# Kernel optimization log

Measured on AMD Instinct MI355X. Metric: run time of the kernel, lower is better.

## Reference

```python
import jax, jax.numpy as jnp
import numpy as np

N, C, H, W = 4, 128, 64, 64


def setup_inputs() -> dict:
    key = jax.random.key(0)
    ks = jax.random.split(key, 4)
    s = 1.0 / np.sqrt(C).astype(np.float32)  # conv2d default-init scale
    return {
        "x": jax.random.normal(ks[0], (N, C, H, W), dtype=jnp.float32),
        "Wq": jax.random.normal(ks[1], (C, C), dtype=jnp.float32) * s,
        "bq": jnp.zeros((C,), dtype=jnp.float32),
        "Wk": jax.random.normal(ks[2], (C, C), dtype=jnp.float32) * s,
        "bk": jnp.zeros((C,), dtype=jnp.float32),
        "Wv": jax.random.normal(ks[3], (C, C), dtype=jnp.float32) * s,
        "bv": jnp.zeros((C,), dtype=jnp.float32),
    }


def reference(x, Wq, bq, Wk, bk, Wv, bv):
    n, c, h, w = x.shape
    xf = x.reshape(n, c, h * w)  # [N, C, L], L = H*W
    # 1x1 convs == per-pixel channel mixing
    q = jnp.einsum('oc,ncl->nol', Wq, xf) + bq[:, None]
    k = jnp.einsum('oc,ncl->nol', Wk, xf) + bk[:, None]
    v = jnp.einsum('oc,ncl->nol', Wv, xf) + bv[:, None]
    # scores[l, m] = sum_c k[c,l] * q[c,m]  (matmul(k^T, q))
    scale = jnp.asarray(1.0 / np.sqrt(c), x.dtype)
    scores = jnp.einsum('ncl,ncm->nlm', k, q) * scale  # [N, L, L]
    temp = jax.nn.softmax(scores, axis=-1)
    attn = jnp.einsum('ncl,nlm->ncm', v, temp)  # [N, C, L]
    return x + attn.reshape(n, c, h, w)
```

## Files before the change

kernel.cpp:

```cpp
#include <hip/hip_runtime.h>
#include <hip/hip_bf16.h>
#include <stdint.h>

#define NB 4
#define CH 128
#define LL 4096

typedef __attribute__((ext_vector_type(8))) short short8;
typedef __attribute__((ext_vector_type(4))) short short4b;
typedef __attribute__((ext_vector_type(4))) float floatx4;
typedef __attribute__((ext_vector_type(16))) float floatx16;


static __device__ __forceinline__ short f2bf(float f) {
    uint32_t u = __float_as_uint(f);
    u += 0x7fffu + ((u >> 16) & 1u);
    return (short)(u >> 16);
}

__global__ __launch_bounds__(256) void wprep_kernel(
    const float* __restrict__ Wq, const float* __restrict__ Wk,
    const float* __restrict__ Wv, short* __restrict__ Wf)
{
    const int g = blockIdx.x * 256 + threadIdx.x;
    const int mat = g >> 14;
    const int rem = g & 16383;
    const int o   = rem >> 7;
    const int c   = rem & 127;
    const float* W = (mat == 0) ? Wq : (mat == 1) ? Wk : Wv;
    float v = W[o * CH + c];
    if (mat == 1) v *= 0.08838834764831845f;
    Wf[(size_t)mat * 16384 + (o >> 4) * 2048 + (c >> 5) * 512
       + ((c >> 3) & 3) * 128 + (o & 15) * 8 + (c & 7)] = f2bf(v);
}

__global__ __launch_bounds__(256) void proj_kernel(
    const float* __restrict__ x, const short* __restrict__ Wf,
    const float* __restrict__ bq, const float* __restrict__ bk,
    const float* __restrict__ bv,
    short* __restrict__ Qf, short* __restrict__ Kf, short* __restrict__ Vp)
{
    const int b    = blockIdx.x;
    const int n    = b >> 7;
    const int lt   = b & 127;
    const int l0   = lt << 5;
    const int tid  = threadIdx.x;
    const int wave = tid >> 6;
    const int lane = tid & 63;
    const int quad = lane >> 4;
    const int mc   = lane & 15;

    __shared__ short Xb[32][136];

    {
        const int sl = tid & 31;
        const int cg = tid >> 5;
        const float* xp = x + ((size_t)n * CH + cg * 16) * LL + l0 + sl;
        short8 buf;
        #pragma unroll
        for (int i = 0; i < 16; ++i) {
            buf[i & 7] = f2bf(xp[(size_t)i * LL]);
            if ((i & 7) == 7)
                *(short8*)(void*)&Xb[sl][cg * 16 + (i & 8)] = buf;
        }
    }
    __syncthreads();

    const int lt2 = wave >> 1;
    const int oh  = wave & 1;
    const int gt  = lt * 2 + lt2;

    short8 xf[4];
    #pragma unroll
    for (int s = 0; s < 4; ++s)
        xf[s] = *(const short8*)(const void*)&Xb[lt2 * 16 + mc][32 * s + quad * 8];

    const size_t obase = ((size_t)n * 256 + gt) * 2048;

    #pragma unroll
    for (int mat = 0; mat < 3; ++mat) {
        const short* Wm = Wf + (size_t)mat * 16384;
        const float* bb = (mat == 0) ? bq : (mat == 1) ? bk : bv;
        const float bscale = (mat == 1) ? 0.08838834764831845f : 1.0f;
        #pragma unroll
        for (int ot = oh * 4; ot < oh * 4 + 4; ++ot) {
            floatx4 acc = {0.f, 0.f, 0.f, 0.f};
            #pragma unroll
            for (int s = 0; s < 4; ++s)
                acc = __builtin_amdgcn_mfma_f32_16x16x32_bf16(
                    *(const short8*)(const void*)(Wm + ot * 2048 + s * 512 + lane * 8),
                    xf[s], acc, 0, 0, 0);
            const int c0 = ot * 16 + 4 * quad;
            if (mat < 2) {
                short4b pv;
                #pragma unroll
                for (int r = 0; r < 4; ++r)
                    pv[r] = f2bf(acc[r] + bb[c0 + r] * bscale);
                short* dst = ((mat == 0) ? Qf : Kf) + obase
                           + (c0 >> 5) * 512 + ((c0 >> 3) & 3) * 128
                           + mc * 8 + (c0 & 7);
                *(short4b*)(void*)dst = pv;
            } else {
                #pragma unroll
                for (int r = 0; r < 4; ++r)
                    Vp[obase + (c0 + r) * 16 + mc] = f2bf(acc[r] + bb[c0 + r]);
            }
        }
    }
}

__global__ __launch_bounds__(256) void rowsum_kernel(
    const short* __restrict__ Qf, const short* __restrict__ Kf,
    float* __restrict__ Dsum)
{
    const int b    = blockIdx.x;
    const int n    = b >> 7;
    const int tp   = b & 127;
    const int wave = threadIdx.x >> 6;
    const int lane = threadIdx.x & 63;
    const int quad = lane >> 4;
    const int mc   = lane & 15;

    const short* Kb = Kf + ((size_t)n * 256 + tp * 2) * 2048 + lane * 8;
    short8 kf[2][4];
    #pragma unroll
    for (int t = 0; t < 2; ++t)
        #pragma unroll
        for (int s = 0; s < 4; ++s)
            kf[t][s] = *(const short8*)(const void*)(Kb + t * 2048 + s * 512);

    const short* Qn = Qf + (size_t)n * 524288 + (size_t)wave * 64 * 2048 + lane * 8;
    float rs[2][4] = {{0.f,0.f,0.f,0.f},{0.f,0.f,0.f,0.f}};

    for (int i = 0; i < 64; i += 2) {
        floatx4 a[2][2];
        #pragma unroll
        for (int t = 0; t < 2; ++t)
            #pragma unroll
            for (int j = 0; j < 2; ++j) a[t][j] = (floatx4){0.f,0.f,0.f,0.f};
        #pragma unroll
        for (int s = 0; s < 4; ++s) {
            const short8 q0 = *(const short8*)(const void*)(Qn + (size_t)i * 2048 + s * 512);
            const short8 q1 = *(const short8*)(const void*)(Qn + (size_t)(i + 1) * 2048 + s * 512);
            #pragma unroll
            for (int t = 0; t < 2; ++t) {
                a[t][0] = __builtin_amdgcn_mfma_f32_16x16x32_bf16(kf[t][s], q0, a[t][0], 0, 0, 0);
                a[t][1] = __builtin_amdgcn_mfma_f32_16x16x32_bf16(kf[t][s], q1, a[t][1], 0, 0, 0);
            }
        }
        #pragma unroll
        for (int t = 0; t < 2; ++t)
            #pragma unroll
            for (int j = 0; j < 2; ++j)
                #pragma unroll
                for (int r = 0; r < 4; ++r) rs[t][r] += __expf(a[t][j][r]);
    }

    #pragma unroll
    for (int t = 0; t < 2; ++t) {
        #pragma unroll
        for (int r = 0; r < 4; ++r) {
            float v = rs[t][r];
            v += __shfl_xor(v, 1);
            v += __shfl_xor(v, 2);
            v += __shfl_xor(v, 4);
            v += __shfl_xor(v, 8);
            rs[t][r] = v;
        }
        if (mc == 0) {
            #pragma unroll
            for (int r = 0; r < 4; ++r)
                atomicAdd(&Dsum[(size_t)n * LL + (tp * 2 + t) * 16 + quad * 4 + r], rs[t][r]);
        }
    }
}

__global__ __launch_bounds__(1024) void attn_out_kernel(
    const short* __restrict__ Qf, const short* __restrict__ Kf,
    const short* __restrict__ Vp, const float* __restrict__ Dsum,
    const float* __restrict__ x, float* __restrict__ out)
{
    const int b    = blockIdx.x;
    const int n    = b >> 6;
    const int m0   = (b & 63) << 6;
    const int tid  = threadIdx.x;
    const int wave = tid >> 6;
    const int lane = tid & 63;
    const int quad = lane >> 4;
    const int mc   = lane & 15;
    const int l32  = lane & 31;
    const int h    = lane >> 5;
    const int ct   = wave & 3;
    const int mh   = (wave >> 2) & 1;
    const int kh   = wave >> 3;

    __shared__ short P[2][64][264];
    __shared__ float Rbuf[4][2][64][16];

    const short* Qn  = Qf + (size_t)n * 524288;
    const short* Kn  = Kf + (size_t)n * 524288;
    const short* Vpn = Vp + (size_t)n * 524288;
    const float* Dn  = Dsum + (size_t)n * LL;

    floatx16 acc;
    #pragma unroll
    for (int r = 0; r < 16; ++r) acc[r] = 0.f;

    for (int step = 0; step < 16; ++step) {
        const int lb = step << 8;
        const int p  = step & 1;

        short8 kfr[4];
        #pragma unroll
        for (int s = 0; s < 4; ++s)
            kfr[s] = *(const short8*)(const void*)(
                Kn + (size_t)(step * 16 + wave) * 2048 + s * 512 + lane * 8);
        const floatx4 ds = *(const floatx4*)(const void*)(Dn + lb + 16 * wave + quad * 4);
        float d[4];
        #pragma unroll
        for (int r = 0; r < 4; ++r) d[r] = 1.0f / ds[r];

        #pragma unroll
        for (int mst = 0; mst < 4; ++mst) {
            floatx4 sa = {0.f, 0.f, 0.f, 0.f};
            #pragma unroll
            for (int s = 0; s < 4; ++s) {
                const short8 qfr = *(const short8*)(const void*)(
                    Qn + (size_t)((m0 >> 4) + mst) * 2048 + s * 512 + lane * 8);
                sa = __builtin_amdgcn_mfma_f32_16x16x32_bf16(kfr[s], qfr, sa, 0, 0, 0);
            }
            short4b pv;
            #pragma unroll
            for (int r = 0; r < 4; ++r) pv[r] = f2bf(__expf(sa[r]) * d[r]);
            *(short4b*)(void*)&P[p][16 * mst + mc][16 * wave + quad * 4] = pv;
        }
        __syncthreads();

        #pragma unroll
        for (int i = 0; i < 8; ++i) {
            const int kc = kh * 8 + i;
            const short8 vf = *(const short8*)(const void*)(
                Vpn + (size_t)((lb >> 4) + kc) * 2048 + (32 * ct + l32) * 16 + 8 * h);
            const short8 pf = *(const short8*)(const void*)&P[p][32 * mh + l32][16 * kc + 8 * h];
            acc = __builtin_amdgcn_mfma_f32_32x32x16_bf16(vf, pf, acc, 0, 0, 0);
        }
    }

    __syncthreads();
    if (kh == 1)
        *(floatx16*)(void*)&Rbuf[ct][mh][lane][0] = acc;
    __syncthreads();
    if (kh == 0) {
        const floatx16 o = *(const floatx16*)(const void*)&Rbuf[ct][mh][lane][0];
        #pragma unroll
        for (int r = 0; r < 16; ++r) {
            const int c = 32 * ct + (r & 3) + 8 * (r >> 2) + 4 * h;
            const int m = m0 + 32 * mh + l32;
            const size_t idx = ((size_t)n * CH + c) * LL + m;
            out[idx] = x[idx] + acc[r] + o[r];
        }
    }
}

extern "C" void kernel_launch(void* const* d_in, const int* in_sizes, int n_in,
                              void* d_out, int out_size, void* d_ws, size_t ws_size,
                              hipStream_t stream) {
    (void)in_sizes; (void)n_in; (void)out_size; (void)ws_size;
    const float* x  = (const float*)d_in[0];
    const float* Wq = (const float*)d_in[1];
    const float* bq = (const float*)d_in[2];
    const float* Wk = (const float*)d_in[3];
    const float* bk = (const float*)d_in[4];
    const float* Wv = (const float*)d_in[5];
    const float* bv = (const float*)d_in[6];
    float* out = (float*)d_out;

    char* ws = (char*)d_ws;
    short* Qf = (short*)(ws);
    short* Kf = (short*)(ws + 4194304);
    short* Vp = (short*)(ws + 8388608);
    float* Ds = (float*)(ws + 12582912);
    short* Wf = (short*)(ws + 12582912 + 65536);

    hipMemsetAsync(Ds, 0, 65536, stream);
    wprep_kernel<<<192, 256, 0, stream>>>(Wq, Wk, Wv, Wf);
    proj_kernel<<<512, 256, 0, stream>>>(x, Wf, bq, bk, bv, Qf, Kf, Vp);
    rowsum_kernel<<<512, 256, 0, stream>>>(Qf, Kf, Ds);
    attn_out_kernel<<<256, 1024, 0, stream>>>(Qf, Kf, Vp, Ds, x, out);
}
```

Baseline: 176.1 us.

## Fold softmax normalization into V, drop weight-prep kernel and memset

Removes the separate weight-prep kernel by converting fp32 weights to bf16 inside the projection kernel. Instead of atomically accumulating row sums and dividing in the attention kernel, the rowsum kernel reduces its partial sums in shared memory, computes reciprocals, and writes a pre-scaled copy of V. The attention kernel then uses unnormalized exp scores and hoists the Q fragments into registers outside the step loop. This cuts two launches, the memset and the atomics, at the cost of an extra V pass, redundant weight conversion per block, and higher register pressure in the attention kernel.

```diff
diff --git a/kernel.cpp b/kernel.cpp
--- a/kernel.cpp
+++ b/kernel.cpp
@@ -17,27 +17,15 @@
     u += 0x7fffu + ((u >> 16) & 1u);
     return (short)(u >> 16);
 }
-
-__global__ __launch_bounds__(256) void wprep_kernel(
-    const float* __restrict__ Wq, const float* __restrict__ Wk,
-    const float* __restrict__ Wv, short* __restrict__ Wf)
-{
-    const int g = blockIdx.x * 256 + threadIdx.x;
-    const int mat = g >> 14;
-    const int rem = g & 16383;
-    const int o   = rem >> 7;
-    const int c   = rem & 127;
-    const float* W = (mat == 0) ? Wq : (mat == 1) ? Wk : Wv;
-    float v = W[o * CH + c];
-    if (mat == 1) v *= 0.08838834764831845f;
-    Wf[(size_t)mat * 16384 + (o >> 4) * 2048 + (c >> 5) * 512
-       + ((c >> 3) & 3) * 128 + (o & 15) * 8 + (c & 7)] = f2bf(v);
+static __device__ __forceinline__ float bf2f(short s) {
+    return __uint_as_float(((uint32_t)(uint16_t)s) << 16);
 }
 
 __global__ __launch_bounds__(256) void proj_kernel(
-    const float* __restrict__ x, const short* __restrict__ Wf,
-    const float* __restrict__ bq, const float* __restrict__ bk,
-    const float* __restrict__ bv,
+    const float* __restrict__ x,
+    const float* __restrict__ Wq, const float* __restrict__ bq,
+    const float* __restrict__ Wk, const float* __restrict__ bk,
+    const float* __restrict__ Wv, const float* __restrict__ bv,
     short* __restrict__ Qf, short* __restrict__ Kf, short* __restrict__ Vp)
 {
     const int b    = blockIdx.x;
@@ -76,26 +64,35 @@
         xf[s] = *(const short8*)(const void*)&Xb[lt2 * 16 + mc][32 * s + quad * 8];
 
     const size_t obase = ((size_t)n * 256 + gt) * 2048;
+    const float scale = 0.08838834764831845f;
 
     #pragma unroll
     for (int mat = 0; mat < 3; ++mat) {
-        const short* Wm = Wf + (size_t)mat * 16384;
+        const float* Wm = (mat == 0) ? Wq : (mat == 1) ? Wk : Wv;
         const float* bb = (mat == 0) ? bq : (mat == 1) ? bk : bv;
-        const float bscale = (mat == 1) ? 0.08838834764831845f : 1.0f;
+        const float wscale = (mat == 1) ? scale : 1.0f;
         #pragma unroll
         for (int ot = oh * 4; ot < oh * 4 + 4; ++ot) {
             floatx4 acc = {0.f, 0.f, 0.f, 0.f};
             #pragma unroll
-            for (int s = 0; s < 4; ++s)
-                acc = __builtin_amdgcn_mfma_f32_16x16x32_bf16(
-                    *(const short8*)(const void*)(Wm + ot * 2048 + s * 512 + lane * 8),
-                    xf[s], acc, 0, 0, 0);
+            for (int s = 0; s < 4; ++s) {
+                const float* wp = Wm + (ot * 16 + mc) * CH + 32 * s + quad * 8;
+                const floatx4 w0 = *(const floatx4*)(const void*)(wp);
+                const floatx4 w1 = *(const floatx4*)(const void*)(wp + 4);
+                short8 wf;
+                #pragma unroll
+                for (int j = 0; j < 4; ++j) {
+                    wf[j]     = f2bf(w0[j] * wscale);
+                    wf[4 + j] = f2bf(w1[j] * wscale);
+                }
+                acc = __builtin_amdgcn_mfma_f32_16x16x32_bf16(wf, xf[s], acc, 0, 0, 0);
+            }
             const int c0 = ot * 16 + 4 * quad;
             if (mat < 2) {
                 short4b pv;
                 #pragma unroll
                 for (int r = 0; r < 4; ++r)
-                    pv[r] = f2bf(acc[r] + bb[c0 + r] * bscale);
+                    pv[r] = f2bf(acc[r] + bb[c0 + r] * wscale);
                 short* dst = ((mat == 0) ? Qf : Kf) + obase
                            + (c0 >> 5) * 512 + ((c0 >> 3) & 3) * 128
                            + mc * 8 + (c0 & 7);
@@ -111,15 +108,19 @@
 
 __global__ __launch_bounds__(256) void rowsum_kernel(
     const short* __restrict__ Qf, const short* __restrict__ Kf,
-    float* __restrict__ Dsum)
+    const short* __restrict__ Vp, short* __restrict__ Vs)
 {
     const int b    = blockIdx.x;
     const int n    = b >> 7;
     const int tp   = b & 127;
-    const int wave = threadIdx.x >> 6;
-    const int lane = threadIdx.x & 63;
+    const int tid  = threadIdx.x;
+    const int wave = tid >> 6;
+    const int lane = tid & 63;
     const int quad = lane >> 4;
     const int mc   = lane & 15;
+
+    __shared__ float Db[4][32];
+    __shared__ float Dr[32];
 
     const short* Kb = Kf + ((size_t)n * 256 + tp * 2) * 2048 + lane * 8;
     short8 kf[2][4];
@@ -170,14 +171,28 @@
         if (mc == 0) {
             #pragma unroll
             for (int r = 0; r < 4; ++r)
-                atomicAdd(&Dsum[(size_t)n * LL + (tp * 2 + t) * 16 + quad * 4 + r], rs[t][r]);
-        }
+                Db[wave][t * 16 + quad * 4 + r] = rs[t][r];
+        }
+    }
+    __syncthreads();
+    if (tid < 32)
+        Dr[tid] = 1.0f / (Db[0][tid] + Db[1][tid] + Db[2][tid] + Db[3][tid]);
+    __syncthreads();
+
+    const short* vsrc = Vp + ((size_t)n * 256 + tp * 2) * 2048;
+    short*       vdst = Vs + ((size_t)n * 256 + tp * 2) * 2048;
+    #pragma unroll
+    for (int k = 0; k < 16; ++k) {
+        const int i = k * 256 + tid;
+        const int tile = i >> 11;
+        const int li   = i & 15;
+        vdst[i] = f2bf(bf2f(vsrc[i]) * Dr[tile * 16 + li]);
     }
 }
 
 __global__ __launch_bounds__(1024) void attn_out_kernel(
     const short* __restrict__ Qf, const short* __restrict__ Kf,
-    const short* __restrict__ Vp, const float* __restrict__ Dsum,
+    const short* __restrict__ Vs,
     const float* __restrict__ x, float* __restrict__ out)
 {
     const int b    = blockIdx.x;
@@ -199,8 +214,15 @@
 
     const short* Qn  = Qf + (size_t)n * 524288;
     const short* Kn  = Kf + (size_t)n * 524288;
-    const short* Vpn = Vp + (size_t)n * 524288;
-    const float* Dn  = Dsum + (size_t)n * LL;
+    const short* Vpn = Vs + (size_t)n * 524288;
+
+    short8 qf[4][4];
+    #pragma unroll
+    for (int mst = 0; mst < 4; ++mst)
+        #pragma unroll
+        for (int s = 0; s < 4; ++s)
+            qf[mst][s] = *(const short8*)(const void*)(
+                Qn + (size_t)((m0 >> 4) + mst) * 2048 + s * 512 + lane * 8);
 
     floatx16 acc;
     #pragma unroll
@@ -215,23 +237,16 @@
         for (int s = 0; s < 4; ++s)
             kfr[s] = *(const short8*)(const void*)(
                 Kn + (size_t)(step * 16 + wave) * 2048 + s * 512 + lane * 8);
-        const floatx4 ds = *(const floatx4*)(const void*)(Dn + lb + 16 * wave + quad * 4);
-        float d[4];
-        #pragma unroll
-        for (int r = 0; r < 4; ++r) d[r] = 1.0f / ds[r];
 
         #pragma unroll
         for (int mst = 0; mst < 4; ++mst) {
             floatx4 sa = {0.f, 0.f, 0.f, 0.f};
             #pragma unroll
-            for (int s = 0; s < 4; ++s) {
-                const short8 qfr = *(const short8*)(const void*)(
-                    Qn + (size_t)((m0 >> 4) + mst) * 2048 + s * 512 + lane * 8);
-                sa = __builtin_amdgcn_mfma_f32_16x16x32_bf16(kfr[s], qfr, sa, 0, 0, 0);
-            }
+            for (int s = 0; s < 4; ++s)
+                sa = __builtin_amdgcn_mfma_f32_16x16x32_bf16(kfr[s], qf[mst][s], sa, 0, 0, 0);
             short4b pv;
             #pragma unroll
-            for (int r = 0; r < 4; ++r) pv[r] = f2bf(__expf(sa[r]) * d[r]);
+            for (int r = 0; r < 4; ++r) pv[r] = f2bf(__expf(sa[r]));
             *(short4b*)(void*)&P[p][16 * mst + mc][16 * wave + quad * 4] = pv;
         }
         __syncthreads();
@@ -279,12 +294,9 @@
     short* Qf = (short*)(ws);
     short* Kf = (short*)(ws + 4194304);
     short* Vp = (short*)(ws + 8388608);
-    float* Ds = (float*)(ws + 12582912);
-    short* Wf = (short*)(ws + 12582912 + 65536);
-
-    hipMemsetAsync(Ds, 0, 65536, stream);
-    wprep_kernel<<<192, 256, 0, stream>>>(Wq, Wk, Wv, Wf);
-    proj_kernel<<<512, 256, 0, stream>>>(x, Wf, bq, bk, bv, Qf, Kf, Vp);
-    rowsum_kernel<<<512, 256, 0, stream>>>(Qf, Kf, Ds);
-    attn_out_kernel<<<256, 1024, 0, stream>>>(Qf, Kf, Vp, Ds, x, out);
-}
+    short* Vs = (short*)(ws + 12582912);
+
+    proj_kernel<<<512, 256, 0, stream>>>(x, Wq, bq, Wk, bk, Wv, bv, Qf, Kf, Vp);
+    rowsum_kernel<<<512, 256, 0, stream>>>(Qf, Kf, Vp, Vs);
+    attn_out_kernel<<<256, 1024, 0, stream>>>(Qf, Kf, Vs, x, out);
+}
```

After: 182.2 us. +3.5%, slower.
